# Kernel optimization log

Measured on AMD Instinct MI355X. Metric: run time of the kernel, lower is better.

Reference implementation:

```python
import jax, jax.numpy as jnp
import numpy as np

TWO_PI = 2.0 * np.pi
ALPHA = 0.65
KSIZE = (3, 3, 3)   # (kOr, kH, kW)
ITERS = 1
BN_EPS = 1e-5


def _interp(v, dy, dx):
    """Bilinear sample of v[b,c,o, y+dy[o], x+dx[o]], border-clamped.
    v: [B,C,Or,H,W]; dy, dx: [Or] float per-orientation constant shifts."""
    H, W = v.shape[3], v.shape[4]
    y0 = jnp.floor(dy); fy = dy - y0; y0 = y0.astype(jnp.int32)
    iy = jnp.arange(H)[None, :] + y0[:, None]                      # [Or,H]
    g0 = jnp.take_along_axis(v, jnp.clip(iy, 0, H - 1)[None, None, :, :, None], axis=3)
    g1 = jnp.take_along_axis(v, jnp.clip(iy + 1, 0, H - 1)[None, None, :, :, None], axis=3)
    fyb = fy[None, None, :, None, None]
    v = (1.0 - fyb) * g0 + fyb * g1
    x0 = jnp.floor(dx); fx = dx - x0; x0 = x0.astype(jnp.int32)
    ix = jnp.arange(W)[None, :] + x0[:, None]                      # [Or,W]
    h0 = jnp.take_along_axis(v, jnp.clip(ix, 0, W - 1)[None, None, :, None, :], axis=4)
    h1 = jnp.take_along_axis(v, jnp.clip(ix + 1, 0, W - 1)[None, None, :, None, :], axis=4)
    fxb = fx[None, None, :, None, None]
    return (1.0 - fxb) * h0 + fxb * h1


def _convection(u, g0):
    """out[b,c,p] = u[b,c, p . g0[c]^{-1}] via trilinear resampling.
    Sample point: ((x,y) - R(theta - th0)@(x0,y0), theta - th0), theta periodic."""
    Or = u.shape[2]
    def one(uc, g):  # uc: [B,Or,H,W], g = (x0, y0, th0)
        x0, y0, th0 = g[0], g[1], g[2]
        t = th0 * Or / TWO_PI
        i = jnp.floor(t); f = t - i; i = i.astype(jnp.int32)
        # periodic linear interpolation along orientation axis
        v = (1.0 - f) * jnp.roll(uc, i, axis=1) + f * jnp.roll(uc, i + 1, axis=1)
        a = jnp.arange(Or, dtype=u.dtype) * (TWO_PI / Or) - th0
        dx = -(jnp.cos(a) * x0 - jnp.sin(a) * y0)
        dy = -(jnp.sin(a) * x0 + jnp.cos(a) * y0)
        return _interp(v[:, None], dy, dx)[:, 0]
    return jax.vmap(one, in_axes=(1, 0), out_axes=1)(u, g0)


def _se2_log(qx, qy, dth):
    """Exact SE(2) logarithm coordinates (c1,c2,c3) of group offset (qx,qy,dth)."""
    if abs(dth) < 1e-9:
        return qx, qy, dth
    h = 0.5 * dth
    cot = np.cos(h) / np.sin(h)
    return h * (qx * cot + qy), h * (-qx + qy * cot), dth


def _morph(u, metric, dilate):
    """Fractional morphological dilation (max of u(p.q) - k(q)) or erosion
    (min of u(p.q) + k(q)) with left-invariant Riemannian kernel
    k_c(q) = nu_a * d_c(q)^{2a/(2a-1)}, d_c^2 = (m0*c1)^2+(m1*c2)^2+(m2*c3)^2."""
    kOr, kH, kW = KSIZE
    Or = u.shape[2]
    thetas = jnp.arange(Or, dtype=u.dtype) * (TWO_PI / Or)
    p = 2.0 * ALPHA / (2.0 * ALPHA - 1.0)
    nu = (2.0 * ALPHA - 1.0) * (2.0 * ALPHA) ** (-p)
    out = None
    for qt in range(-(kOr // 2), kOr // 2 + 1):
        dth = qt * TWO_PI / Or
        for qy in range(-(kH // 2), kH // 2 + 1):
            for qx in range(-(kW // 2), kW // 2 + 1):
                c1, c2, c3 = _se2_log(float(qx), float(qy), dth)
                s = (metric[:, 0] * c1) ** 2 + (metric[:, 1] * c2) ** 2 + (metric[:, 2] * c3) ** 2
                k = nu * s ** (p / 2.0)                       # [C]
                # left-invariant shift: spatial offset rotated by theta_o
                dxo = jnp.cos(thetas) * qx - jnp.sin(thetas) * qy
                dyo = jnp.sin(thetas) * qx + jnp.cos(thetas) * qy
                val = _interp(jnp.roll(u, -qt, axis=2), dyo, dxo)
                kb = k[None, :, None, None, None]
                cand = val - kb if dilate else val + kb
                if out is None:
                    out = cand
                else:
                    out = jnp.maximum(out, cand) if dilate else jnp.minimum(out, cand)
    return out


def setup_inputs() -> dict:
    key = jax.random.key(0)
    ks = jax.random.split(key, 5)
    B, Cin, Cout, Or, H, W = 4, 8, 16, 8, 128, 128
    x = jax.random.normal(ks[0], (B, Cin, Or, H, W), dtype=jnp.float32)
    g0 = 0.5 * jax.random.normal(ks[1], (Cin, 3), dtype=jnp.float32)
    lo, hi = 1.4 / 3.0, 0.7 * 3.0   # reset_parameters range for metric params
    metric_dil = jax.random.uniform(ks[2], (Cin, 3), minval=lo, maxval=hi, dtype=jnp.float32)
    metric_ero = jax.random.uniform(ks[3], (Cin, 3), minval=lo, maxval=hi, dtype=jnp.float32)
    bound = 0.25  # kaiming_uniform(a=sqrt(5)) bound for [8,16] weight
    weight = jax.random.uniform(ks[4], (Cin, Cout), minval=-bound, maxval=bound, dtype=jnp.float32)
    gamma = jnp.ones((Cout,), jnp.float32)
    beta = jnp.zeros((Cout,), jnp.float32)
    return dict(x=x, g0=g0, metric_dil=metric_dil, metric_ero=metric_ero,
                weight=weight, gamma=gamma, beta=beta)


def reference(x, g0, metric_dil, metric_ero, weight, gamma, beta):
    u = x
    for _ in range(ITERS):
        u = _convection(u, g0)
        u = _morph(u, metric_dil, dilate=True)
        u = _morph(u, metric_ero, dilate=False)
    # channel mixing: [B,Cin,Or,H,W] x [Cin,Cout] -> [B,Cout,Or,H,W]
    y = jnp.einsum('bcohw,cd->bdohw', u, weight)
    # BatchNorm3d (training mode): per-channel stats over (B,Or,H,W)
    m = y.mean(axis=(0, 2, 3, 4), keepdims=True)
    v = y.var(axis=(0, 2, 3, 4), keepdims=True)
    yh = (y - m) * jax.lax.rsqrt(v + BN_EPS)
    return yh * gamma[None, :, None, None, None] + beta[None, :, None, None, None]
```

## Files before the change

kernel.cpp:

```cpp
#include <hip/hip_runtime.h>
#include <math.h>
#include <utility>

#define B 4
#define CIN 8
#define COUT 16
#define OR_ 8
#define H_ 128
#define W_ 128
#define HW 16384
#define PLANE HW
#define CH_STR (OR_*HW)
#define BATCH_STR (CIN*CH_STR)
#define NELEM (B*BATCH_STR)
#define NPOS (B*OR_*HW)
#define NB_RED 256

#define TILE 16
#define CBR 24
#define DBR 20
#define STR4 11
#define CB_PL4 (CBR*STR4)
#define DB_PL4 (DBR*STR4)

typedef __attribute__((ext_vector_type(4))) float f4;

__host__ __device__ constexpr double m_cos(int o) {
  const double r = 0.70710678118654752440;
  const double t[8] = {1.0, r, 0.0, -r, -1.0, -r, 0.0, r};
  return t[o];
}
__host__ __device__ constexpr double m_sin(int o) {
  const double r = 0.70710678118654752440;
  const double t[8] = {0.0, r, 1.0, r, 0.0, -r, -1.0, -r};
  return t[o];
}
__host__ __device__ constexpr double tap_dx(int o, int j) {
  return m_cos(o)*(j % 3 - 1) - m_sin(o)*(j / 3 - 1);
}
__host__ __device__ constexpr double tap_dy(int o, int j) {
  return m_sin(o)*(j % 3 - 1) + m_cos(o)*(j / 3 - 1);
}
__host__ __device__ constexpr int ifloor(double v) {
  int i = (int)v;
  return ((double)i > v) ? i - 1 : i;
}
__host__ __device__ constexpr int tap_ix(int o, int j) { return ifloor(tap_dx(o, j)); }
__host__ __device__ constexpr int tap_iy(int o, int j) { return ifloor(tap_dy(o, j)); }
__host__ __device__ constexpr float tap_fx(int o, int j) { return (float)(tap_dx(o, j) - tap_ix(o, j)); }
__host__ __device__ constexpr float tap_fy(int o, int j) { return (float)(tap_dy(o, j) - tap_iy(o, j)); }
__host__ __device__ constexpr float corner_w(int o, int j, int dyb, int dxb) {
  float fy = tap_fy(o, j), fx = tap_fx(o, j);
  return (dyb ? fy : 1.0f - fy) * (dxb ? fx : 1.0f - fx);
}
__host__ __device__ constexpr int corner_r(int o, int j, int dyb) { return tap_iy(o, j) + dyb + 2; }
__host__ __device__ constexpr int corner_c(int o, int j, int i, int dxb) { return i + tap_ix(o, j) + dxb + 2; }
__host__ __device__ constexpr bool row_used(int o, int r) {
  for (int j = 0; j < 9; ++j)
    for (int dyb = 0; dyb < 2; ++dyb)
      for (int dxb = 0; dxb < 2; ++dxb)
        if (corner_w(o, j, dyb, dxb) != 0.0f && corner_r(o, j, dyb) == r)
          return true;
  return false;
}

template<int N> struct Rep {
  template<class F> __device__ __forceinline__ static void run(F&& f) {
    Rep<N-1>::run(f);
    f(std::integral_constant<int, N-1>{});
  }
};
template<> struct Rep<0> {
  template<class F> __device__ __forceinline__ static void run(F&&) {}
};

template<int O, int DIL, int PLF4>
__device__ __forceinline__ void morph_tile_lds(const f4* __restrict__ sm,
                                               const float* __restrict__ kt,
                                               int row, int gc4, float acc[4]) {
  Rep<3>::run([&](auto qc) {
    constexpr int qti = decltype(qc)::value;
    const f4* p = sm + ((O + qti + 7) & 7) * PLF4 + row * STR4 + gc4;
    f4 wv[5][2];
    Rep<5>::run([&](auto rc) {
      constexpr int r = decltype(rc)::value;
      if constexpr (row_used(O, r)) {
        wv[r][0] = p[r*STR4];
        wv[r][1] = p[r*STR4 + 1];
      }
    });
    Rep<9>::run([&](auto jc) {
      constexpr int j = decltype(jc)::value;
      float k = kt[qti*9 + j];
      float base = DIL ? -k : k;
      Rep<4>::run([&](auto ic) {
        constexpr int i = decltype(ic)::value;
        float v = base;
        Rep<4>::run([&](auto cc2) {
          constexpr int dyb = decltype(cc2)::value >> 1, dxb = decltype(cc2)::value & 1;
          constexpr float Wgt = corner_w(O, j, dyb, dxb);
          if constexpr (Wgt != 0.0f) {
            constexpr int R = corner_r(O, j, dyb);
            constexpr int C = corner_c(O, j, i, dxb);
            v = fmaf(Wgt, wv[R][C >> 2][C & 3], v);
          }
        });
        acc[i] = DIL ? fmaxf(acc[i], v) : fminf(acc[i], v);
      });
    });
  });
}

template<int O>
__device__ __forceinline__ void dil_compute(const f4* __restrict__ sm,
                                            const float* __restrict__ kt, int lane,
                                            float accA[4], float accB[4]) {
  int rA = lane / 5, cA = lane - rA*5;
  morph_tile_lds<O, 1, CB_PL4>(sm, kt, rA, cA, accA);
  if (lane < 36) {
    int g = lane + 64;
    int rB = g / 5, cB = g - rB*5;
    morph_tile_lds<O, 1, CB_PL4>(sm, kt, rB, cB, accB);
  }
}

template<int O>
__device__ __forceinline__ void ero_compute(const f4* __restrict__ sm,
                                            const float* __restrict__ kt, int lane,
                                            float* __restrict__ dst) {
  int pr = lane >> 2, pc = lane & 3;
  float acc[4] = {INFINITY, INFINITY, INFINITY, INFINITY};
  morph_tile_lds<O, 0, DB_PL4>(sm, kt, pr, pc, acc);
  f4 v = {acc[0], acc[1], acc[2], acc[3]};
  *(f4*)(dst + pr*W_ + pc*4) = v;
}

__global__ __launch_bounds__(512, 4)
void fused_kernel(const float* __restrict__ x,
                  const float* __restrict__ g0,
                  const float* __restrict__ mdil,
                  const float* __restrict__ mero,
                  float* __restrict__ u3) {
  __shared__ f4 smem[8*CB_PL4];
  __shared__ float kdilL[27], keroL[27];
  __shared__ float cw00[8], cw01[8], cw10[8], cw11[8], ccf[1];
  __shared__ int   cply1[8], cply2[8], ciy0[8], cix0[8];

  int blk = blockIdx.x;
  int tx = blk & 7, ty = (blk >> 3) & 7, c = (blk >> 6) & 7, b = blk >> 9;
  int h0 = ty*TILE, w0 = tx*TILE;
  int t = threadIdx.x;
  int wid = t >> 6, lane = t & 63;

  {
    const double TWO_PI = 6.283185307179586476925286766559;
    if (t < 54) {
      const double P  = 2.0*0.65/(2.0*0.65 - 1.0);
      const double NU = (2.0*0.65 - 1.0)*pow(2.0*0.65, -P);
      int which = t / 27;
      int j = t % 27;
      int qt = j/9 - 1;
      int qy = (j/3)%3 - 1;
      int qx = j%3 - 1;
      double dth = qt * (TWO_PI/OR_);
      double c1, c2, c3;
      if (qt == 0) { c1 = qx; c2 = qy; c3 = 0.0; }
      else {
        double h = 0.5*dth;
        double cot = cos(h)/sin(h);
        c1 = h*(qx*cot + qy);
        c2 = h*(-qx + qy*cot);
        c3 = dth;
      }
      const float* m = which ? mero : mdil;
      double a0 = (double)m[c*3+0]*c1;
      double a1 = (double)m[c*3+1]*c2;
      double a2 = (double)m[c*3+2]*c3;
      double s = a0*a0 + a1*a1 + a2*a2;
      float k = (float)(NU * pow(s, P*0.5));
      (which ? keroL : kdilL)[j] = k;
    } else if (t >= 64 && t < 72) {
      int o = t - 64;
      float x0 = g0[c*3+0], y0 = g0[c*3+1], th0 = g0[c*3+2];
      float a = (float)(o*(TWO_PI/OR_)) - th0;
      float ca = cosf(a), sa = sinf(a);
      float dxv = -(ca*x0 - sa*y0);
      float dyv = -(sa*x0 + ca*y0);
      float fy0 = floorf(dyv), fx0 = floorf(dxv);
      float fy = dyv - fy0, fx = dxv - fx0;
      ciy0[o] = (int)fy0;
      cix0[o] = (int)fx0;
      cw00[o] = (1.f-fy)*(1.f-fx);
      cw01[o] = (1.f-fy)*fx;
      cw10[o] = fy*(1.f-fx);
      cw11[o] = fy*fx;
      float tt = th0 * (float)(OR_/TWO_PI);
      float fi = floorf(tt);
      int ci = (int)fi;
      cply1[o] = (o - ci) & 7;
      cply2[o] = (o - ci - 1) & 7;
      if (o == 0) ccf[0] = tt - fi;
    }
  }
  __syncthreads();

  {
    const int o = wid;
    const float* p1 = x + b*BATCH_STR + c*CH_STR + cply1[o]*PLANE;
    const float* p2 = x + b*BATCH_STR + c*CH_STR + cply2[o]*PLANE;
    const int iy0 = ciy0[o], ix0 = cix0[o];
    const float w00 = cw00[o], w01 = cw01[o], w10 = cw10[o], w11 = cw11[o];
    const float cfv = ccf[0];
    float* cbf = (float*)(smem + o*CB_PL4);
    #pragma unroll
    for (int it = 0; it < 3; ++it) {
      int q = lane + it*64;
      if (q < 144) {
        int r = q / 6, cq = q - r*6;
        int gr = h0 - 4 + r;
        int gc4 = w0 - 4 + cq*4;
        int iy = gr + iy0, ix = gc4 + ix0;
        bool ok = (gr >= 0) & (gr <= 127) & (gc4 >= 0) & (gc4+3 <= 127)
                & (iy >= 0) & (iy <= 126) & (ix >= 0) & (ix+4 <= 127);
        if (ok) {
          const float* q1 = p1 + iy*W_ + ix;
          const float* q2 = p2 + iy*W_ + ix;
          float a[5], bb[5], cc[5], dd[5];
          #pragma unroll
          for (int k = 0; k < 5; ++k) {
            a[k] = q1[k]; bb[k] = q1[W_+k]; cc[k] = q2[k]; dd[k] = q2[W_+k];
          }
          f4 res;
          #pragma unroll
          for (int i = 0; i < 4; ++i) {
            float v1 = w00*a[i] + w01*a[i+1] + w10*bb[i] + w11*bb[i+1];
            float v2 = w00*cc[i] + w01*cc[i+1] + w10*dd[i] + w11*dd[i+1];
            res[i] = (1.0f - cfv)*v1 + cfv*v2;
          }
          *(f4*)(cbf + r*44 + cq*4) = res;
        } else {
          int gh = min(max(gr, 0), 127);
          #pragma unroll
          for (int i = 0; i < 4; ++i) {
            int gw = min(max(gc4 + i, 0), 127);
            int yy = gh + iy0, xx = gw + ix0;
            int r0 = min(max(yy, 0), 127), r1 = min(max(yy+1, 0), 127);
            int c0 = min(max(xx, 0), 127), c1 = min(max(xx+1, 0), 127);
            float v1 = w00*p1[r0*W_+c0] + w01*p1[r0*W_+c1] + w10*p1[r1*W_+c0] + w11*p1[r1*W_+c1];
            float v2 = w00*p2[r0*W_+c0] + w01*p2[r0*W_+c1] + w10*p2[r1*W_+c0] + w11*p2[r1*W_+c1];
            cbf[r*44 + cq*4 + i] = (1.0f - cfv)*v1 + cfv*v2;
          }
        }
      }
    }
  }
  __syncthreads();

  float accA[4] = {-INFINITY, -INFINITY, -INFINITY, -INFINITY};
  float accB[4] = {-INFINITY, -INFINITY, -INFINITY, -INFINITY};
  switch (wid) {
    case 0: dil_compute<0>(smem, kdilL, lane, accA, accB); break;
    case 1: dil_compute<1>(smem, kdilL, lane, accA, accB); break;
    case 2: dil_compute<2>(smem, kdilL, lane, accA, accB); break;
    case 3: dil_compute<3>(smem, kdilL, lane, accA, accB); break;
    case 4: dil_compute<4>(smem, kdilL, lane, accA, accB); break;
    case 5: dil_compute<5>(smem, kdilL, lane, accA, accB); break;
    case 6: dil_compute<6>(smem, kdilL, lane, accA, accB); break;
    default: dil_compute<7>(smem, kdilL, lane, accA, accB); break;
  }
  __syncthreads();

  {
    f4* db = smem + wid*DB_PL4;
    int rA = lane / 5, cA = lane - rA*5;
    f4 vA = {accA[0], accA[1], accA[2], accA[3]};
    db[rA*STR4 + cA] = vA;
    if (lane < 36) {
      int g = lane + 64;
      int rB = g / 5, cB = g - rB*5;
      f4 vB = {accB[0], accB[1], accB[2], accB[3]};
      db[rB*STR4 + cB] = vB;
    }
  }
  __syncthreads();

  if ((h0 == 0) | (h0 == 112) | (w0 == 0) | (w0 == 112)) {
    float* df = (float*)smem;
    #pragma unroll
    for (int k2 = 0; k2 < 7; ++k2) {
      int i = t + k2*512;
      if (i < 3200) {
        int o = i / 400, rest = i - o*400;
        int row = rest / 20, col = rest - row*20;
        int vh = h0 - 2 + row, vw = w0 - 2 + col;
        int dr = min(max(vh, 0), 127) - vh;
        int dc = min(max(vw, 0), 127) - vw;
        if ((dr | dc) != 0) {
          df[o*(DB_PL4*4) + row*44 + col] =
            df[o*(DB_PL4*4) + (row + dr)*44 + col + dc];
        }
      }
    }
  }
  __syncthreads();

  {
    float* dst = u3 + ((b*CIN + c)*OR_ + wid)*PLANE + h0*W_ + w0;
    switch (wid) {
      case 0: ero_compute<0>(smem, keroL, lane, dst); break;
      case 1: ero_compute<1>(smem, keroL, lane, dst); break;
      case 2: ero_compute<2>(smem, keroL, lane, dst); break;
      case 3: ero_compute<3>(smem, keroL, lane, dst); break;
      case 4: ero_compute<4>(smem, keroL, lane, dst); break;
      case 5: ero_compute<5>(smem, keroL, lane, dst); break;
      case 6: ero_compute<6>(smem, keroL, lane, dst); break;
      default: ero_compute<7>(smem, keroL, lane, dst); break;
    }
  }
}

__global__ void gram_kernel(const float* __restrict__ u, double* __restrict__ part) {
  int t8 = blockIdx.x*256 + threadIdx.x;
  int hw = (t8 & 2047) << 3;
  int o  = (t8 >> 11) & 7;
  int b  = t8 >> 14;
  const float* base = u + b*BATCH_STR + o*PLANE + hw;
  f4 v0[8], v1[8];
  #pragma unroll
  for (int c = 0; c < 8; c++) {
    v0[c] = *(const f4*)(base + c*CH_STR);
    v1[c] = *(const f4*)(base + c*CH_STR + 4);
  }
  float S[8], G[36];
  #pragma unroll
  for (int c = 0; c < 8; c++)
    S[c] = (v0[c].x + v0[c].y) + (v0[c].z + v0[c].w)
         + (v1[c].x + v1[c].y) + (v1[c].z + v1[c].w);
  {
    int t = 0;
    #pragma unroll
    for (int c = 0; c < 8; c++)
      #pragma unroll
      for (int c2 = c; c2 < 8; c2++) {
        G[t] = v0[c].x*v0[c2].x + v0[c].y*v0[c2].y + v0[c].z*v0[c2].z + v0[c].w*v0[c2].w
             + v1[c].x*v1[c2].x + v1[c].y*v1[c2].y + v1[c].z*v1[c2].z + v1[c].w*v1[c2].w;
        t++;
      }
  }
  __shared__ double lds[4][44];
  int lane = threadIdx.x & 63;
  int wave = threadIdx.x >> 6;
  for (int t = 0; t < 44; t++) {
    double vv = (double)((t < 8) ? S[t] : G[t-8]);
    for (int off = 32; off; off >>= 1) vv += __shfl_down(vv, off);
    if (lane == 0) lds[wave][t] = vv;
  }
  __syncthreads();
  if (threadIdx.x < 44) {
    part[blockIdx.x*44 + threadIdx.x] =
      lds[0][threadIdx.x] + lds[1][threadIdx.x] + lds[2][threadIdx.x] + lds[3][threadIdx.x];
  }
}

__global__ void stats_kernel(const double* __restrict__ part, const float* __restrict__ weight,
                             const float* __restrict__ gamma, const float* __restrict__ beta,
                             float* __restrict__ ss) {
  __shared__ double tot[44];
  int t = threadIdx.x;
  if (t < 352) {
    int cnt = t >> 3, j = t & 7;
    double s = 0.0;
    #pragma unroll 8
    for (int k = 0; k < 32; ++k) s += part[(j + (k << 3))*44 + cnt];
    s += __shfl_down(s, 4);
    s += __shfl_down(s, 2);
    s += __shfl_down(s, 1);
    if (j == 0) tot[cnt] = s;
  }
  __syncthreads();
  if (t < 16) {
    double m = 0.0;
    for (int c = 0; c < 8; c++) m += (double)weight[c*COUT + t] * tot[c];
    double e2 = 0.0;
    int idx = 8;
    for (int c = 0; c < 8; c++)
      for (int c2 = c; c2 < 8; c2++) {
        double wp = (double)weight[c*COUT + t] * (double)weight[c2*COUT + t];
        e2 += (c2 == c ? 1.0 : 2.0) * wp * tot[idx];
        idx++;
      }
    double N = (double)NPOS;
    m /= N; e2 /= N;
    double var = e2 - m*m;
    double inv = rsqrt(var + 1e-5);
    float sc = (float)(inv * (double)gamma[t]);
    ss[t]      = sc;
    ss[16 + t] = beta[t] - (float)m * sc;
  }
}

__global__ void final_kernel(const float* __restrict__ u, const float* __restrict__ weight,
                             const float* __restrict__ ss, float* __restrict__ out) {
  __shared__ float Wsh[8][16];
  __shared__ float scale[16], shift[16];
  int t = threadIdx.x;
  if (t < 128) Wsh[t >> 4][t & 15] = weight[t];
  if (t < 16) { scale[t] = ss[t]; shift[t] = ss[16 + t]; }
  __syncthreads();
  int t4 = blockIdx.x*256 + threadIdx.x;
  int hw = (t4 & 4095) << 2;
  int o  = (t4 >> 12) & 7;
  int b  = t4 >> 15;
  const float* base = u + b*BATCH_STR + o*PLANE + hw;
  f4 v[8];
  #pragma unroll
  for (int c = 0; c < 8; c++) v[c] = *(const f4*)(base + c*CH_STR);
  float* ob = out + b*(COUT*CH_STR) + o*PLANE + hw;
  #pragma unroll
  for (int d = 0; d < 16; d++) {
    f4 y = {0.f, 0.f, 0.f, 0.f};
    #pragma unroll
    for (int c = 0; c < 8; c++) {
      float wv = Wsh[c][d];
      y.x = fmaf(v[c].x, wv, y.x);
      y.y = fmaf(v[c].y, wv, y.y);
      y.z = fmaf(v[c].z, wv, y.z);
      y.w = fmaf(v[c].w, wv, y.w);
    }
    float sc = scale[d], sh = shift[d];
    f4 r = { fmaf(y.x, sc, sh), fmaf(y.y, sc, sh), fmaf(y.z, sc, sh), fmaf(y.w, sc, sh) };
    *(f4*)(ob + d*CH_STR) = r;
  }
}

extern "C" void kernel_launch(void* const* d_in, const int* in_sizes, int n_in,
                              void* d_out, int out_size, void* d_ws, size_t ws_size,
                              hipStream_t stream) {
  const float* x      = (const float*)d_in[0];
  const float* g0     = (const float*)d_in[1];
  const float* mdil   = (const float*)d_in[2];
  const float* mero   = (const float*)d_in[3];
  const float* weight = (const float*)d_in[4];
  const float* gamma  = (const float*)d_in[5];
  const float* beta   = (const float*)d_in[6];
  float* out = (float*)d_out;

  char* ws = (char*)d_ws;
  float*  ss   = (float*)(ws + 8*1024);
  double* part = (double*)(ws + 16*1024);
  float*  u3   = (float*)(ws + (size_t)1*1024*1024);

  fused_kernel<<<B*CIN*64, 512, 0, stream>>>(x, g0, mdil, mero, u3);
  gram_kernel<<<NB_RED, 256, 0, stream>>>(u3, part);
  stats_kernel<<<1, 384, 0, stream>>>(part, weight, gamma, beta, ss);
  final_kernel<<<NPOS/4/256, 256, 0, stream>>>(u3, weight, ss, out);
}
```

Before: 125.3 us.

## Use separate scalar LDS buffers with odd strides and float-precision kernel setup

```diff
diff --git a/kernel.cpp b/kernel.cpp
--- a/kernel.cpp
+++ b/kernel.cpp
@@ -18,10 +18,11 @@
 
 #define TILE 16
 #define CBR 24
+#define CB_S 29
+#define CB_PL (CBR*CB_S)
 #define DBR 20
-#define STR4 11
-#define CB_PL4 (CBR*STR4)
-#define DB_PL4 (DBR*STR4)
+#define DB_S 21
+#define DB_PL (DBR*DB_S)
 
 typedef __attribute__((ext_vector_type(4))) float f4;
 
@@ -74,19 +75,19 @@
   template<class F> __device__ __forceinline__ static void run(F&&) {}
 };
 
-template<int O, int DIL, int PLF4>
-__device__ __forceinline__ void morph_tile_lds(const f4* __restrict__ sm,
+template<int O, int DIL, int PL, int RSTR>
+__device__ __forceinline__ void morph_tile_lds(const float* __restrict__ sm,
                                                const float* __restrict__ kt,
-                                               int row, int gc4, float acc[4]) {
+                                               int row, int gc, float acc[4]) {
   Rep<3>::run([&](auto qc) {
     constexpr int qti = decltype(qc)::value;
-    const f4* p = sm + ((O + qti + 7) & 7) * PLF4 + row * STR4 + gc4;
-    f4 wv[5][2];
+    const float* p = sm + ((O + qti + 7) & 7) * PL + row * RSTR + gc;
+    float win[5][8];
     Rep<5>::run([&](auto rc) {
       constexpr int r = decltype(rc)::value;
       if constexpr (row_used(O, r)) {
-        wv[r][0] = p[r*STR4];
-        wv[r][1] = p[r*STR4 + 1];
+        #pragma unroll
+        for (int k = 0; k < 8; ++k) win[r][k] = p[r*RSTR + k];
       }
     });
     Rep<9>::run([&](auto jc) {
@@ -102,7 +103,7 @@
           if constexpr (Wgt != 0.0f) {
             constexpr int R = corner_r(O, j, dyb);
             constexpr int C = corner_c(O, j, i, dxb);
-            v = fmaf(Wgt, wv[R][C >> 2][C & 3], v);
+            v = fmaf(Wgt, win[R][C], v);
           }
         });
         acc[i] = DIL ? fmaxf(acc[i], v) : fminf(acc[i], v);
@@ -112,27 +113,35 @@
 }
 
 template<int O>
-__device__ __forceinline__ void dil_compute(const f4* __restrict__ sm,
-                                            const float* __restrict__ kt, int lane,
-                                            float accA[4], float accB[4]) {
-  int rA = lane / 5, cA = lane - rA*5;
-  morph_tile_lds<O, 1, CB_PL4>(sm, kt, rA, cA, accA);
+__device__ __forceinline__ void dil_wave(const float* __restrict__ cb, float* __restrict__ db,
+                                         const float* __restrict__ kt, int lane) {
+  {
+    int rA = lane / 5, cA = (lane - rA*5) * 4;
+    float acc[4] = {-INFINITY, -INFINITY, -INFINITY, -INFINITY};
+    morph_tile_lds<O, 1, CB_PL, CB_S>(cb, kt, rA, cA, acc);
+    float* d = db + O*DB_PL + rA*DB_S + cA;
+    #pragma unroll
+    for (int i = 0; i < 4; ++i) d[i] = acc[i];
+  }
   if (lane < 36) {
     int g = lane + 64;
-    int rB = g / 5, cB = g - rB*5;
-    morph_tile_lds<O, 1, CB_PL4>(sm, kt, rB, cB, accB);
+    int rB = g / 5, cB = (g - rB*5) * 4;
+    float acc[4] = {-INFINITY, -INFINITY, -INFINITY, -INFINITY};
+    morph_tile_lds<O, 1, CB_PL, CB_S>(cb, kt, rB, cB, acc);
+    float* d = db + O*DB_PL + rB*DB_S + cB;
+    #pragma unroll
+    for (int i = 0; i < 4; ++i) d[i] = acc[i];
   }
 }
 
 template<int O>
-__device__ __forceinline__ void ero_compute(const f4* __restrict__ sm,
-                                            const float* __restrict__ kt, int lane,
-                                            float* __restrict__ dst) {
-  int pr = lane >> 2, pc = lane & 3;
+__device__ __forceinline__ void ero_wave(const float* __restrict__ db, float* __restrict__ dst,
+                                         const float* __restrict__ kt, int lane) {
+  int pr = lane >> 2, pc = (lane & 3) * 4;
   float acc[4] = {INFINITY, INFINITY, INFINITY, INFINITY};
-  morph_tile_lds<O, 0, DB_PL4>(sm, kt, pr, pc, acc);
+  morph_tile_lds<O, 0, DB_PL, DB_S>(db, kt, pr, pc, acc);
   f4 v = {acc[0], acc[1], acc[2], acc[3]};
-  *(f4*)(dst + pr*W_ + pc*4) = v;
+  *(f4*)(dst + pr*W_ + pc) = v;
 }
 
 __global__ __launch_bounds__(512, 4)
@@ -141,7 +150,8 @@
                   const float* __restrict__ mdil,
                   const float* __restrict__ mero,
                   float* __restrict__ u3) {
-  __shared__ f4 smem[8*CB_PL4];
+  __shared__ float convbuf[8*CB_PL];
+  __shared__ float dilbuf[8*DB_PL];
   __shared__ float kdilL[27], keroL[27];
   __shared__ float cw00[8], cw01[8], cw10[8], cw11[8], ccf[1];
   __shared__ int   cply1[8], cply2[8], ciy0[8], cix0[8];
@@ -153,36 +163,36 @@
   int wid = t >> 6, lane = t & 63;
 
   {
-    const double TWO_PI = 6.283185307179586476925286766559;
+    const float TWO_PI = 6.2831853071795864769f;
     if (t < 54) {
-      const double P  = 2.0*0.65/(2.0*0.65 - 1.0);
-      const double NU = (2.0*0.65 - 1.0)*pow(2.0*0.65, -P);
+      const float P  = 2.0f*0.65f/(2.0f*0.65f - 1.0f);
+      const float NU = (2.0f*0.65f - 1.0f)*powf(2.0f*0.65f, -P);
       int which = t / 27;
       int j = t % 27;
       int qt = j/9 - 1;
       int qy = (j/3)%3 - 1;
       int qx = j%3 - 1;
-      double dth = qt * (TWO_PI/OR_);
-      double c1, c2, c3;
-      if (qt == 0) { c1 = qx; c2 = qy; c3 = 0.0; }
+      float c1, c2, c3;
+      if (qt == 0) { c1 = (float)qx; c2 = (float)qy; c3 = 0.0f; }
       else {
-        double h = 0.5*dth;
-        double cot = cos(h)/sin(h);
+        float dth = qt * (TWO_PI/OR_);
+        float h = 0.5f*dth;
+        float cot = cosf(h)/sinf(h);
         c1 = h*(qx*cot + qy);
         c2 = h*(-qx + qy*cot);
         c3 = dth;
       }
       const float* m = which ? mero : mdil;
-      double a0 = (double)m[c*3+0]*c1;
-      double a1 = (double)m[c*3+1]*c2;
-      double a2 = (double)m[c*3+2]*c3;
-      double s = a0*a0 + a1*a1 + a2*a2;
-      float k = (float)(NU * pow(s, P*0.5));
+      float a0 = m[c*3+0]*c1;
+      float a1 = m[c*3+1]*c2;
+      float a2 = m[c*3+2]*c3;
+      float s = a0*a0 + a1*a1 + a2*a2;
+      float k = NU * powf(s, P*0.5f);
       (which ? keroL : kdilL)[j] = k;
     } else if (t >= 64 && t < 72) {
       int o = t - 64;
       float x0 = g0[c*3+0], y0 = g0[c*3+1], th0 = g0[c*3+2];
-      float a = (float)(o*(TWO_PI/OR_)) - th0;
+      float a = (float)o*(TWO_PI/OR_) - th0;
       float ca = cosf(a), sa = sinf(a);
       float dxv = -(ca*x0 - sa*y0);
       float dyv = -(sa*x0 + ca*y0);
@@ -194,7 +204,7 @@
       cw01[o] = (1.f-fy)*fx;
       cw10[o] = fy*(1.f-fx);
       cw11[o] = fy*fx;
-      float tt = th0 * (float)(OR_/TWO_PI);
+      float tt = th0 * ((float)OR_/TWO_PI);
       float fi = floorf(tt);
       int ci = (int)fi;
       cply1[o] = (o - ci) & 7;
@@ -211,7 +221,7 @@
     const int iy0 = ciy0[o], ix0 = cix0[o];
     const float w00 = cw00[o], w01 = cw01[o], w10 = cw10[o], w11 = cw11[o];
     const float cfv = ccf[0];
-    float* cbf = (float*)(smem + o*CB_PL4);
+    float* cbf = convbuf + o*CB_PL;
     #pragma unroll
     for (int it = 0; it < 3; ++it) {
       int q = lane + it*64;
@@ -222,22 +232,24 @@
         int iy = gr + iy0, ix = gc4 + ix0;
         bool ok = (gr >= 0) & (gr <= 127) & (gc4 >= 0) & (gc4+3 <= 127)
                 & (iy >= 0) & (iy <= 126) & (ix >= 0) & (ix+4 <= 127);
+        float* dst = cbf + r*CB_S + cq*4;
         if (ok) {
           const float* q1 = p1 + iy*W_ + ix;
           const float* q2 = p2 + iy*W_ + ix;
-          float a[5], bb[5], cc[5], dd[5];
-          #pragma unroll
-          for (int k = 0; k < 5; ++k) {
-            a[k] = q1[k]; bb[k] = q1[W_+k]; cc[k] = q2[k]; dd[k] = q2[W_+k];
-          }
-          f4 res;
+          f4 A0 = *(const f4*)q1;       float A4 = q1[4];
+          f4 B0 = *(const f4*)(q1+W_);  float B4 = q1[W_+4];
+          f4 C0 = *(const f4*)q2;       float C4 = q2[4];
+          f4 D0 = *(const f4*)(q2+W_);  float D4 = q2[W_+4];
+          float a[5] = {A0.x, A0.y, A0.z, A0.w, A4};
+          float bb[5] = {B0.x, B0.y, B0.z, B0.w, B4};
+          float cc[5] = {C0.x, C0.y, C0.z, C0.w, C4};
+          float dd[5] = {D0.x, D0.y, D0.z, D0.w, D4};
           #pragma unroll
           for (int i = 0; i < 4; ++i) {
             float v1 = w00*a[i] + w01*a[i+1] + w10*bb[i] + w11*bb[i+1];
             float v2 = w00*cc[i] + w01*cc[i+1] + w10*dd[i] + w11*dd[i+1];
-            res[i] = (1.0f - cfv)*v1 + cfv*v2;
+            dst[i] = (1.0f - cfv)*v1 + cfv*v2;
           }
-          *(f4*)(cbf + r*44 + cq*4) = res;
         } else {
           int gh = min(max(gr, 0), 127);
           #pragma unroll
@@ -248,7 +260,7 @@
             int c0 = min(max(xx, 0), 127), c1 = min(max(xx+1, 0), 127);
             float v1 = w00*p1[r0*W_+c0] + w01*p1[r0*W_+c1] + w10*p1[r1*W_+c0] + w11*p1[r1*W_+c1];
             float v2 = w00*p2[r0*W_+c0] + w01*p2[r0*W_+c1] + w10*p2[r1*W_+c0] + w11*p2[r1*W_+c1];
-            cbf[r*44 + cq*4 + i] = (1.0f - cfv)*v1 + cfv*v2;
+            dst[i] = (1.0f - cfv)*v1 + cfv*v2;
           }
         }
       }
@@ -256,36 +268,19 @@
   }
   __syncthreads();
 
-  float accA[4] = {-INFINITY, -INFINITY, -INFINITY, -INFINITY};
-  float accB[4] = {-INFINITY, -INFINITY, -INFINITY, -INFINITY};
   switch (wid) {
-    case 0: dil_compute<0>(smem, kdilL, lane, accA, accB); break;
-    case 1: dil_compute<1>(smem, kdilL, lane, accA, accB); break;
-    case 2: dil_compute<2>(smem, kdilL, lane, accA, accB); break;
-    case 3: dil_compute<3>(smem, kdilL, lane, accA, accB); break;
-    case 4: dil_compute<4>(smem, kdilL, lane, accA, accB); break;
-    case 5: dil_compute<5>(smem, kdilL, lane, accA, accB); break;
-    case 6: dil_compute<6>(smem, kdilL, lane, accA, accB); break;
-    default: dil_compute<7>(smem, kdilL, lane, accA, accB); break;
-  }
-  __syncthreads();
-
-  {
-    f4* db = smem + wid*DB_PL4;
-    int rA = lane / 5, cA = lane - rA*5;
-    f4 vA = {accA[0], accA[1], accA[2], accA[3]};
-    db[rA*STR4 + cA] = vA;
-    if (lane < 36) {
-      int g = lane + 64;
-      int rB = g / 5, cB = g - rB*5;
-      f4 vB = {accB[0], accB[1], accB[2], accB[3]};
-      db[rB*STR4 + cB] = vB;
-    }
+    case 0: dil_wave<0>(convbuf, dilbuf, kdilL, lane); break;
+    case 1: dil_wave<1>(convbuf, dilbuf, kdilL, lane); break;
+    case 2: dil_wave<2>(convbuf, dilbuf, kdilL, lane); break;
+    case 3: dil_wave<3>(convbuf, dilbuf, kdilL, lane); break;
+    case 4: dil_wave<4>(convbuf, dilbuf, kdilL, lane); break;
+    case 5: dil_wave<5>(convbuf, dilbuf, kdilL, lane); break;
+    case 6: dil_wave<6>(convbuf, dilbuf, kdilL, lane); break;
+    default: dil_wave<7>(convbuf, dilbuf, kdilL, lane); break;
   }
   __syncthreads();
 
   if ((h0 == 0) | (h0 == 112) | (w0 == 0) | (w0 == 112)) {
-    float* df = (float*)smem;
     #pragma unroll
     for (int k2 = 0; k2 < 7; ++k2) {
       int i = t + k2*512;
@@ -296,8 +291,8 @@
         int dr = min(max(vh, 0), 127) - vh;
         int dc = min(max(vw, 0), 127) - vw;
         if ((dr | dc) != 0) {
-          df[o*(DB_PL4*4) + row*44 + col] =
-            df[o*(DB_PL4*4) + (row + dr)*44 + col + dc];
+          dilbuf[o*DB_PL + row*DB_S + col] =
+            dilbuf[o*DB_PL + (row + dr)*DB_S + col + dc];
         }
       }
     }
@@ -307,14 +302,14 @@
   {
     float* dst = u3 + ((b*CIN + c)*OR_ + wid)*PLANE + h0*W_ + w0;
     switch (wid) {
-      case 0: ero_compute<0>(smem, keroL, lane, dst); break;
-      case 1: ero_compute<1>(smem, keroL, lane, dst); break;
-      case 2: ero_compute<2>(smem, keroL, lane, dst); break;
-      case 3: ero_compute<3>(smem, keroL, lane, dst); break;
-      case 4: ero_compute<4>(smem, keroL, lane, dst); break;
-      case 5: ero_compute<5>(smem, keroL, lane, dst); break;
-      case 6: ero_compute<6>(smem, keroL, lane, dst); break;
-      default: ero_compute<7>(smem, keroL, lane, dst); break;
+      case 0: ero_wave<0>(dilbuf, dst, keroL, lane); break;
+      case 1: ero_wave<1>(dilbuf, dst, keroL, lane); break;
+      case 2: ero_wave<2>(dilbuf, dst, keroL, lane); break;
+      case 3: ero_wave<3>(dilbuf, dst, keroL, lane); break;
+      case 4: ero_wave<4>(dilbuf, dst, keroL, lane); break;
+      case 5: ero_wave<5>(dilbuf, dst, keroL, lane); break;
+      case 6: ero_wave<6>(dilbuf, dst, keroL, lane); break;
+      default: ero_wave<7>(dilbuf, dst, keroL, lane); break;
     }
   }
 }
```

Result: slower. 134.3 us (+7.2%).
